# Kernel tuning notes

Hardware: AMD Instinct MI355X
Metric: run time of the kernel (lower is better)

## Reference

```python
import jax, jax.numpy as jnp
import numpy as np

B, T, C, H = 2, 2048, 1024, 16
D = C // H  # head_dim = 64


def setup_inputs() -> dict:
    key = jax.random.key(0)
    ks = jax.random.split(key, 5)
    s = 1.0 / np.sqrt(C)
    return {
        "x": jax.random.normal(ks[0], (B, T, C), jnp.float32),
        "Wq": jax.random.normal(ks[1], (C, C), jnp.float32) * s,
        "bq": jnp.zeros((C,), jnp.float32),
        "Wk": jax.random.normal(ks[2], (C, C), jnp.float32) * s,
        "bk": jnp.zeros((C,), jnp.float32),
        "Wv": jax.random.normal(ks[3], (C, C), jnp.float32) * s,
        "bv": jnp.zeros((C,), jnp.float32),
        "Wo": jax.random.normal(ks[4], (C, C), jnp.float32) * s,
        "bo": jnp.zeros((C,), jnp.float32),
    }


def reference(x, Wq, bq, Wk, bk, Wv, bv, Wo, bo):
    Bx, Tx, Cx = x.shape
    # torch Linear: y = x @ W.T + b
    q = (x @ Wq.T + bq).reshape(Bx, Tx, H, D).transpose(0, 2, 1, 3)  # [B,H,T,D]
    k = (x @ Wk.T + bk).reshape(Bx, Tx, H, D).transpose(0, 2, 1, 3)
    v = (x @ Wv.T + bv).reshape(Bx, Tx, H, D).transpose(0, 2, 1, 3)
    att = jnp.einsum("bhqd,bhkd->bhqk", q, k) / np.sqrt(D).astype(np.float32)
    mask = jnp.tril(jnp.ones((Tx, Tx), bool))  # causal mask [T,T]
    att = jnp.where(mask, att, -jnp.inf)
    att = jax.nn.softmax(att, axis=-1)
    out = jnp.einsum("bhqk,bhkd->bhqd", att, v)
    out = out.transpose(0, 2, 1, 3).reshape(Bx, Tx, Cx)
    return out @ Wo.T + bo
```

## Files before the change

### kernel.cpp

```cpp
#include <hip/hip_runtime.h>
#include <hip/hip_bf16.h>

#define B_ 2
#define T_ 2048
#define C_ 1024
#define H_ 16
#define D_ 64

typedef unsigned short u16;
typedef __bf16 bf16x8 __attribute__((ext_vector_type(8)));
typedef float floatx4 __attribute__((ext_vector_type(4)));

__device__ __forceinline__ float bf2f(u16 u) {
  union { unsigned int i; float f; } x; x.i = ((unsigned int)u) << 16; return x.f;
}
__device__ __forceinline__ u16 f2bf(float f) {
  union { float f; unsigned int i; } x; x.f = f;
  unsigned int r = x.i + 0x7fffu + ((x.i >> 16) & 1u);
  return (u16)(r >> 16);
}

__device__ __forceinline__ unsigned cvtpk(float lo, float hi) {
  unsigned r;
  asm("v_cvt_pk_bf16_f32 %0, %1, %2" : "=v"(r) : "v"(lo), "v"(hi));
  return r;
}

__device__ __forceinline__ void gld16(void* lds, const void* g) {
  __builtin_amdgcn_global_load_lds(
      (const __attribute__((address_space(1))) unsigned int*)g,
      (__attribute__((address_space(3))) unsigned int*)lds, 16, 0, 0);
}

#define NXF4 1048576
#define NWF4 262144

__global__ __launch_bounds__(256) void cvt_all(
    const float* __restrict__ x,  const float* __restrict__ Wq,
    const float* __restrict__ Wk, const float* __restrict__ Wv,
    const float* __restrict__ Wo, u16* __restrict__ dst_base)
{
  const int i = blockIdx.x * 256 + threadIdx.x;
  const float* src; size_t off;
  if (i < NXF4)               { src = x;  off = i; }
  else if (i < NXF4 + NWF4)   { src = Wq; off = i - NXF4; }
  else if (i < NXF4 + 2*NWF4) { src = Wk; off = i - (NXF4 + NWF4); }
  else if (i < NXF4 + 3*NWF4) { src = Wv; off = i - (NXF4 + 2*NWF4); }
  else                        { src = Wo; off = i - (NXF4 + 3*NWF4); }
  float4 f = ((const float4*)src)[off];
  ushort4 o;
  o.x = f2bf(f.x); o.y = f2bf(f.y); o.z = f2bf(f.z); o.w = f2bf(f.w);
  ((ushort4*)dst_base)[i] = o;
}

#define QSCALE 0.1803368801111f

#define PBAR()                                                \
  do {                                                        \
    asm volatile("" ::: "memory");                            \
    __builtin_amdgcn_s_barrier();                             \
    asm volatile("s_waitcnt lgkmcnt(0)" ::: "memory");        \
  } while (0)

#define EBAR()                                                \
  do {                                                        \
    asm volatile("" ::: "memory");                            \
    __builtin_amdgcn_s_barrier();                             \
    asm volatile("" ::: "memory");                            \
  } while (0)

__global__ __launch_bounds__(512, 2) void gemm_qkv8(
    const u16* __restrict__ X, const u16* __restrict__ Wb,
    const float* __restrict__ b0, const float* __restrict__ b1,
    const float* __restrict__ b2,
    u16* __restrict__ Yq, u16* __restrict__ Yk, u16* __restrict__ Yv)
{
  __shared__ __align__(16) u16 L[57344];

  const int tid  = threadIdx.x;
  const int lane = tid & 63;
  const int m16  = lane & 15;
  const int q4   = lane >> 4;
  const int wv   = tid >> 6;
  const int wm   = wv >> 2;
  const int wn   = wv & 3;

  const int bid = blockIdx.x;
  const int xcd = bid & 7;
  const int idx = bid >> 3;
  const int bx  = (xcd & 3) * 4 + (idx & 3);
  const int by  = (xcd >> 2) * 8 + (idx >> 2);

  const u16* Abase  = X  + (size_t)bx * 256 * C_;
  const u16* Bbase  = Wb + (size_t)by * 192 * C_;
  const u16* A1base = Abase + (size_t)128 * C_;

  const int rB  = tid >> 3;
  const int s0 = tid,       r0 = rB;
  const int s1 = tid + 512, r1 = 64 + rB;
  const int k0a = ((tid & 7) ^ (rB & 7)) * 8;

#define STAGE_A(dsthalf, srcrows, kofs)                                       \
  do {                                                                        \
    gld16(&(dsthalf)[s0 * 8], (srcrows) + (size_t)r0 * C_ + (kofs) + k0a);    \
    gld16(&(dsthalf)[s1 * 8], (srcrows) + (size_t)r1 * C_ + (kofs) + k0a);    \
  } while (0)

#define STAGE_BL(dstB, srcrows, kofs, l)                                      \
  gld16(&(dstB)[((l) * 512 + tid) * 8],                                       \
        (srcrows) + (size_t)((l) * 64 + rB) * C_ + (kofs) + k0a)

  u16* buf0 = L;
  u16* buf1 = L + 28672;

  STAGE_BL(buf0 + 16384, Bbase, 0, 0);
  STAGE_BL(buf0 + 16384, Bbase, 0, 1);
  STAGE_BL(buf0 + 16384, Bbase, 0, 2);
  STAGE_A (buf0,         Abase,  0);
  STAGE_A (buf0 + 8192,  A1base, 0);
  STAGE_BL(buf1 + 16384, Bbase, 64, 0);
  STAGE_BL(buf1 + 16384, Bbase, 64, 1);
  STAGE_A (buf1,         Abase, 64);
  asm volatile("s_waitcnt vmcnt(4)" ::: "memory");
  __builtin_amdgcn_s_barrier();
  asm volatile("" ::: "memory");

  floatx4 acc[8][3] = {};

  const int a0off = m16 * 64 + ((q4      ^ (lane & 7)) * 8);
  const int a1off = m16 * 64 + (((q4 + 4) ^ (lane & 7)) * 8);
  const int bro   = wn * 3072;

  for (int i = 0; i < 16; ++i) {
    u16* buf  = (i & 1) ? buf1 : buf0;
    u16* bufn = (i & 1) ? buf0 : buf1;
    const u16* Ah = buf + wm * 8192;
    const u16* Bh = buf + 16384;
    const bool p1 = (i + 1) < 16;
    const bool p2 = (i + 2) < 16;
    const int  k1 = (i + 1) * 64;
    const int  k2 = (i + 2) * 64;

    bf16x8 a[4][2], bA[2][2], bB[2];

#pragma unroll
    for (int f = 0; f < 4; ++f) {
      a[f][0] = *(const bf16x8*)&Ah[f * 1024 + a0off];
      a[f][1] = *(const bf16x8*)&Ah[f * 1024 + a1off];
    }
#pragma unroll
    for (int g = 0; g < 2; ++g) {
      bA[g][0] = *(const bf16x8*)&Bh[bro + g * 1024 + a0off];
      bA[g][1] = *(const bf16x8*)&Bh[bro + g * 1024 + a1off];
    }
    if (p1) STAGE_A(bufn + 8192, A1base, k1);
    PBAR();
    __builtin_amdgcn_s_setprio(1);
#pragma unroll
    for (int f = 0; f < 4; ++f)
#pragma unroll
      for (int g = 0; g < 2; ++g) {
        acc[f][g] = __builtin_amdgcn_mfma_f32_16x16x32_bf16(a[f][0], bA[g][0], acc[f][g], 0, 0, 0);
        acc[f][g] = __builtin_amdgcn_mfma_f32_16x16x32_bf16(a[f][1], bA[g][1], acc[f][g], 0, 0, 0);
      }
    __builtin_amdgcn_s_setprio(0);
    EBAR();

    bB[0] = *(const bf16x8*)&Bh[bro + 2048 + a0off];
    bB[1] = *(const bf16x8*)&Bh[bro + 2048 + a1off];
    if (p1) STAGE_BL(bufn + 16384, Bbase, k1, 2);
    PBAR();
    __builtin_amdgcn_s_setprio(1);
#pragma unroll
    for (int f = 0; f < 4; ++f) {
      acc[f][2] = __builtin_amdgcn_mfma_f32_16x16x32_bf16(a[f][0], bB[0], acc[f][2], 0, 0, 0);
      acc[f][2] = __builtin_amdgcn_mfma_f32_16x16x32_bf16(a[f][1], bB[1], acc[f][2], 0, 0, 0);
    }
    __builtin_amdgcn_s_setprio(0);
    EBAR();

#pragma unroll
    for (int f = 0; f < 4; ++f) {
      a[f][0] = *(const bf16x8*)&Ah[4096 + f * 1024 + a0off];
      a[f][1] = *(const bf16x8*)&Ah[4096 + f * 1024 + a1off];
    }
    if (p2) {
      STAGE_BL(buf + 16384, Bbase, k2, 0);
      STAGE_BL(buf + 16384, Bbase, k2, 1);
    }
    PBAR();
    __builtin_amdgcn_s_setprio(1);
#pragma unroll
    for (int f = 0; f < 4; ++f) {
      acc[4 + f][2] = __builtin_amdgcn_mfma_f32_16x16x32_bf16(a[f][0], bB[0], acc[4 + f][2], 0, 0, 0);
      acc[4 + f][2] = __builtin_amdgcn_mfma_f32_16x16x32_bf16(a[f][1], bB[1], acc[4 + f][2], 0, 0, 0);
    }
    __builtin_amdgcn_s_setprio(0);
    EBAR();

    if (p2) STAGE_A(buf, Abase, k2);
    PBAR();
    __builtin_amdgcn_s_setprio(1);
#pragma unroll
    for (int f = 0; f < 4; ++f)
#pragma unroll
      for (int g = 0; g < 2; ++g) {
        acc[4 + f][g] = __builtin_amdgcn_mfma_f32_16x16x32_bf16(a[f][0], bA[g][0], acc[4 + f][g], 0, 0, 0);
        acc[4 + f][g] = __builtin_amdgcn_mfma_f32_16x16x32_bf16(a[f][1], bA[g][1], acc[4 + f][g], 0, 0, 0);
      }
    __builtin_amdgcn_s_setprio(0);
    asm volatile("" ::: "memory");
    if (p2) asm volatile("s_waitcnt vmcnt(4)" ::: "memory");
    else    asm volatile("s_waitcnt vmcnt(0)" ::: "memory");
    __builtin_amdgcn_s_barrier();
    asm volatile("" ::: "memory");
  }

  const int mbase = bx * 256 + wm * 128 + q4 * 4;
#pragma unroll
  for (int nf = 0; nf < 3; ++nf) {
    const int nzg = by * 192 + wn * 48 + nf * 16 + m16;
    const int z  = nzg >> 10;
    const int nl = nzg & 1023;
    const int h = nl >> 6, d = nl & (D_ - 1);
    const float bv = (z == 0 ? b0 : z == 1 ? b1 : b2)[nl];
    if (z == 2) {
#pragma unroll
      for (int mf = 0; mf < 8; ++mf) {
        const int m  = mbase + mf * 16;
        const int bb = m >> 11, t = m & (T_ - 1);
        ushort4 pk;
        pk.x = f2bf(acc[mf][nf][0] + bv);
        pk.y = f2bf(acc[mf][nf][1] + bv);
        pk.z = f2bf(acc[mf][nf][2] + bv);
        pk.w = f2bf(acc[mf][nf][3] + bv);
        *(ushort4*)&Yv[(((size_t)bb * H_ + h) * D_ + d) * T_ + t] = pk;
      }
    } else {
      u16* Y = z ? Yk : Yq;
      const float sc = z ? 1.0f : QSCALE;
#pragma unroll
      for (int mf = 0; mf < 8; ++mf) {
        const int m  = mbase + mf * 16;
        const int bb = m >> 11, tq = m & (T_ - 1);
#pragma unroll
        for (int r = 0; r < 4; ++r) {
          Y[(((size_t)bb * H_ + h) * T_ + (tq + r)) * D_ + d] =
              f2bf((acc[mf][nf][r] + bv) * sc);
        }
      }
    }
  }
}

__global__ __launch_bounds__(256) void gemm_out(
    const u16* __restrict__ X, const u16* __restrict__ W,
    const float* __restrict__ bias, float* __restrict__ Yf)
{
  const int K = C_, N = C_;
  __shared__ __align__(16) u16 As[128 * 32];
  __shared__ __align__(16) u16 Bs[128 * 32];

  const int tid  = threadIdx.x;
  const int wv   = tid >> 6;
  const int lane = tid & 63;
  const int mcol = lane & 15;
  const int quad = lane >> 4;
  const int wr = wv >> 1, wc = wv & 1;
  const int m0 = blockIdx.x * 128;
  const int n0 = blockIdx.y * 128;

  const int srow = tid >> 2;
  const int scol = (tid & 3) * 8;
  const u16* xp0 = X + (size_t)(m0 + srow) * K + scol;
  const u16* xp1 = xp0 + (size_t)64 * K;
  const u16* wp0 = W + (size_t)(n0 + srow) * K + scol;
  const u16* wp1 = wp0 + (size_t)64 * K;

  floatx4 acc[4][4] = {};

  for (int k0 = 0; k0 < K; k0 += 32) {
    gld16(&As[tid * 8],        xp0 + k0);
    gld16(&As[2048 + tid * 8], xp1 + k0);
    gld16(&Bs[tid * 8],        wp0 + k0);
    gld16(&Bs[2048 + tid * 8], wp1 + k0);
    __syncthreads();

    bf16x8 a[4], b[4];
#pragma unroll
    for (int rf = 0; rf < 4; ++rf)
      a[rf] = *(const bf16x8*)&As[(wr * 64 + rf * 16 + mcol) * 32 + quad * 8];
#pragma unroll
    for (int cf = 0; cf < 4; ++cf)
      b[cf] = *(const bf16x8*)&Bs[(wc * 64 + cf * 16 + mcol) * 32 + quad * 8];
#pragma unroll
    for (int rf = 0; rf < 4; ++rf)
#pragma unroll
      for (int cf = 0; cf < 4; ++cf)
        acc[rf][cf] = __builtin_amdgcn_mfma_f32_16x16x32_bf16(
            a[rf], b[cf], acc[rf][cf], 0, 0, 0);
    __syncthreads();
  }

#pragma unroll
  for (int cf = 0; cf < 4; ++cf) {
    const int n = n0 + wc * 64 + cf * 16 + mcol;
    const float bv = bias[n];
#pragma unroll
    for (int rf = 0; rf < 4; ++rf) {
#pragma unroll
      for (int r = 0; r < 4; ++r) {
        const int m = m0 + wr * 64 + rf * 16 + quad * 4 + r;
        Yf[(size_t)m * N + n] = acc[rf][cf][r] + bv;
      }
    }
  }
}

#define KSB 4096
#define VTB 4096

__global__ __launch_bounds__(256, 5) void attn_flash(
    const u16* __restrict__ Q, const u16* __restrict__ K,
    const u16* __restrict__ Vg, u16* __restrict__ O,
    float* __restrict__ OP, float* __restrict__ LP)
{
  __shared__ __align__(16) u16 Ks[2 * KSB];
  __shared__ __align__(16) u16 Vt[2 * VTB];

  const int tid  = threadIdx.x;
  const int wv   = tid >> 6;
  const int lane = tid & 63;
  const int mcol = lane & 15;
  const int quad = lane >> 4;

  const int bx = blockIdx.x;
  const int bh = bx & 31;
  const int t  = bx >> 5;
  const int iq = (t < 16) ? 31 - t : 47 - t;
  const bool pc = (t < 32);
  const int j0 = (t >= 16 && t < 32) ? 16 : 0;
  const int j1 = (t < 16) ? 15 : iq;
  const int ti = pc ? ((bh * 16 + (iq - 16)) * 2 + (j0 ? 1 : 0)) : 0;

  const size_t base  = (size_t)bh * T_ * D_;
  const size_t vbase = (size_t)bh * D_ * T_;
  const int b = bh >> 4, h = bh & (H_ - 1);

  bf16x8 vones;
  {
    const u16 ov = (mcol == 0) ? (u16)0x3F80 : (u16)0;
    union { u16 s[8]; bf16x8 v; } tmp;
#pragma unroll
    for (int i = 0; i < 8; ++i) tmp.s[i] = ov;
    vones = tmp.v;
  }

  const int srow = lane >> 3;
  const int sg   = (lane & 7) ^ srow;
  const int c0 = wv * 2, c1 = wv * 2 + 1;
  const int sl0 = (quad ^ (mcol & 7)) * 8;

  const size_t koff0 = base + (size_t)(c0 * 8 + srow) * D_ + sg * 8;
  const size_t koff1 = base + (size_t)(c1 * 8 + srow) * D_ + sg * 8;
  const size_t voff0 = vbase + (size_t)(c0 * 8 + srow) * T_ + sg * 8;
  const size_t voff1 = vbase + (size_t)(c1 * 8 + srow) * T_ + sg * 8;

  const u16* qg = Q + base + (size_t)(iq * 64 + wv * 16 + mcol) * D_ + quad * 8;
  const bf16x8 qf0 = *(const bf16x8*)qg;
  const bf16x8 qf1 = *(const bf16x8*)(qg + 32);

  floatx4 oacc[5] = {};

  {
    const size_t kj = (size_t)j0 * 64 * D_;
    const int    vj = j0 * 64;
    gld16(&Ks[c0 * 512 + lane * 8], K  + koff0 + kj);
    gld16(&Ks[c1 * 512 + lane * 8], K  + koff1 + kj);
    gld16(&Vt[c0 * 512 + lane * 8], Vg + voff0 + vj);
    gld16(&Vt[c1 * 512 + lane * 8], Vg + voff1 + vj);
  }

  for (int j = j0; j <= j1; ++j) {
    const int cur = (j - j0) & 1;
    __syncthreads();

    if (j < j1) {
      const int nb = cur ^ 1;
      const size_t kj = (size_t)(j + 1) * 64 * D_;
      const int    vj = (j + 1) * 64;
      gld16(&Ks[nb * KSB + c0 * 512 + lane * 8], K  + koff0 + kj);
      gld16(&Ks[nb * KSB + c1 * 512 + lane * 8], K  + koff1 + kj);
      gld16(&Vt[nb * VTB + c0 * 512 + lane * 8], Vg + voff0 + vj);
      gld16(&Vt[nb * VTB + c1 * 512 + lane * 8], Vg + voff1 + vj);
    }

    const u16* ksb = &Ks[cur * KSB];
    const u16* vtb = &Vt[cur * VTB];

    floatx4 sacc[4] = {};
#pragma unroll
    for (int nt = 0; nt < 4; ++nt) {
      const u16* kr = &ksb[(nt * 16 + mcol) * 64];
      bf16x8 kb0 = *(const bf16x8*)&kr[sl0];
      bf16x8 kb1 = *(const bf16x8*)&kr[sl0 ^ 32];
      sacc[nt] = __builtin_amdgcn_mfma_f32_16x16x32_bf16(kb0, qf0, sacc[nt], 0, 0, 0);
      sacc[nt] = __builtin_amdgcn_mfma_f32_16x16x32_bf16(kb1, qf1, sacc[nt], 0, 0, 0);
    }

    if (j == iq) {
      const int ql = wv * 16 + mcol;
#pragma unroll
      for (int nt = 0; nt < 4; ++nt) {
#pragma unroll
        for (int r = 0; r < 4; ++r)
          if (nt * 16 + quad * 4 + r > ql) sacc[nt][r] = -1e30f;
      }
    }

    unsigned w0[2], w1[2], w2[2], w3[2];
#pragma unroll
    for (int i = 0; i < 2; ++i) {
      w0[i] = cvtpk(exp2f(sacc[0][2*i]), exp2f(sacc[0][2*i+1]));
      w1[i] = cvtpk(exp2f(sacc[1][2*i]), exp2f(sacc[1][2*i+1]));
      w2[i] = cvtpk(exp2f(sacc[2][2*i]), exp2f(sacc[2][2*i+1]));
      w3[i] = cvtpk(exp2f(sacc[3][2*i]), exp2f(sacc[3][2*i+1]));
    }

    union { unsigned u[4]; bf16x8 v; } pa0u, pa1u;
#pragma unroll
    for (int i = 0; i < 2; ++i) {
      unsigned x = w0[i], y = w1[i];
      asm("v_permlane32_swap_b32 %0, %1" : "+v"(x), "+v"(y));
      asm("v_permlane16_swap_b32 %0, %1" : "+v"(x), "+v"(y));
      pa0u.u[i] = x; pa0u.u[i + 2] = y;
      unsigned x2 = w2[i], y2 = w3[i];
      asm("v_permlane32_swap_b32 %0, %1" : "+v"(x2), "+v"(y2));
      asm("v_permlane16_swap_b32 %0, %1" : "+v"(x2), "+v"(y2));
      pa1u.u[i] = x2; pa1u.u[i + 2] = y2;
    }
    const bf16x8 pa0 = pa0u.v;
    const bf16x8 pa1 = pa1u.v;

#pragma unroll
    for (int dt = 0; dt < 4; ++dt) {
      const u16* vr = &vtb[(dt * 16 + mcol) * 64];
      bf16x8 vb0 = *(const bf16x8*)&vr[sl0];
      bf16x8 vb1 = *(const bf16x8*)&vr[sl0 ^ 32];
      oacc[dt] = __builtin_amdgcn_mfma_f32_16x16x32_bf16(pa0, vb0, oacc[dt], 0, 0, 0);
      oacc[dt] = __builtin_amdgcn_mfma_f32_16x16x32_bf16(pa1, vb1, oacc[dt], 0, 0, 0);
    }
    oacc[4] = __builtin_amdgcn_mfma_f32_16x16x32_bf16(pa0, vones, oacc[4], 0, 0, 0);
    oacc[4] = __builtin_amdgcn_mfma_f32_16x16x32_bf16(pa1, vones, oacc[4], 0, 0, 0);
  }

  if (!pc) {
    float invl[4];
#pragma unroll
    for (int r = 0; r < 4; ++r)
      invl[r] = 1.f / __shfl(oacc[4][r], lane & 48);
#pragma unroll
    for (int dt = 0; dt < 4; ++dt) {
      const int c = h * D_ + dt * 16 + mcol;
#pragma unroll
      for (int r = 0; r < 4; ++r) {
        const int tg = iq * 64 + wv * 16 + quad * 4 + r;
        O[((size_t)b * T_ + tg) * C_ + c] = f2bf(oacc[dt][r] * invl[r]);
      }
    }
  } else {
    float* op = OP + (size_t)ti * 4096;
#pragma unroll
    for (int dt = 0; dt < 4; ++dt)
#pragma unroll
      for (int r = 0; r < 4; ++r)
        op[(wv * 16 + quad * 4 + r) * 64 + dt * 16 + mcol] = oacc[dt][r];
    if (mcol == 0) {
#pragma unroll
      for (int r = 0; r < 4; ++r)
        LP[ti * 64 + wv * 16 + quad * 4 + r] = oacc[4][r];
    }
  }
}

__global__ __launch_bounds__(256) void attn_merge(
    const float* __restrict__ OP, const float* __restrict__ LP,
    u16* __restrict__ O)
{
  const int mb = blockIdx.x;
  const int bh = mb & 31, qt = mb >> 5;
  const int iq = 16 + qt;
  const int ti0 = (bh * 16 + qt) * 2;
  const int b = bh >> 4, h = bh & (H_ - 1);
  const int row = threadIdx.x >> 2;
  const int dc  = (threadIdx.x & 3) * 16;

  const float l = LP[ti0 * 64 + row] + LP[(ti0 + 1) * 64 + row];
  const float inv = 1.f / l;
  const float* pa = OP + (size_t)ti0 * 4096 + row * 64 + dc;
  const float* pb = pa + 4096;

  const int tg = iq * 64 + row;
  u16* o = O + ((size_t)b * T_ + tg) * C_ + h * D_ + dc;

  u16 tmp[16];
#pragma unroll
  for (int i = 0; i < 4; ++i) {
    const float4 a4 = ((const float4*)pa)[i];
    const float4 b4 = ((const float4*)pb)[i];
    tmp[i*4 + 0] = f2bf((a4.x + b4.x) * inv);
    tmp[i*4 + 1] = f2bf((a4.y + b4.y) * inv);
    tmp[i*4 + 2] = f2bf((a4.z + b4.z) * inv);
    tmp[i*4 + 3] = f2bf((a4.w + b4.w) * inv);
  }
  *(uint4*)&o[0] = *(const uint4*)&tmp[0];
  *(uint4*)&o[8] = *(const uint4*)&tmp[8];
}

extern "C" void kernel_launch(void* const* d_in, const int* in_sizes, int n_in,
                              void* d_out, int out_size, void* d_ws, size_t ws_size,
                              hipStream_t stream) {
  const float* x  = (const float*)d_in[0];
  const float* Wq = (const float*)d_in[1];
  const float* bq = (const float*)d_in[2];
  const float* Wk = (const float*)d_in[3];
  const float* bk = (const float*)d_in[4];
  const float* Wv = (const float*)d_in[5];
  const float* bv = (const float*)d_in[6];
  const float* Wo = (const float*)d_in[7];
  const float* bo = (const float*)d_in[8];
  float* out = (float*)d_out;

  const size_t NX = (size_t)B_ * T_ * C_;
  const size_t NW = (size_t)C_ * C_;

  u16* xb  = (u16*)d_ws;
  u16* wqb = xb  + NX;
  u16* wkb = wqb + NW;
  u16* wvb = wkb + NW;
  u16* wob = wvb + NW;
  u16* q   = wob + NW;
  u16* k   = q   + NX;
  u16* v   = k   + NX;
  u16* ctx = v   + NX;
  float* opart = (float*)(ctx + NX);
  float* lpart = opart + (size_t)1024 * 4096;

  cvt_all<<<dim3((NXF4 + 4 * NWF4) / 256), 256, 0, stream>>>(x, Wq, Wk, Wv, Wo, xb);

  gemm_qkv8<<<dim3(256), 512, 0, stream>>>(xb, wqb, bq, bk, bv, q, k, v);

  attn_flash<<<dim3(1536), 256, 0, stream>>>(q, k, v, ctx, opart, lpart);

  attn_merge<<<dim3(512), 256, 0, stream>>>(opart, lpart, ctx);

  gemm_out<<<dim3(32, 8), 256, 0, stream>>>(ctx, wob, bo, out);
}
```

Baseline: 183.6 us.

## Enlarge attention query tile to 128 rows with table-driven causal split scheduling

Each attention block now handles 128 query rows, two 16-row sub-tiles per wave, so every K/V tile staged in shared memory feeds twice as many MFMAs. This halves K/V load and barrier traffic per unit of work. A constant lookup table assigns each of 24 chunk slots a query tile and key range, splitting long causal rows into two partials merged later, and the merge kernel is adjusted to match. MFMA sections are wrapped in s_setprio, and occupancy hints drop to 3 blocks per SM, which raises register pressure and shortens the grid to 768 blocks.

```diff
diff --git a/kernel.cpp b/kernel.cpp
--- a/kernel.cpp
+++ b/kernel.cpp
@@ -320,7 +320,12 @@
 #define KSB 4096
 #define VTB 4096
 
-__global__ __launch_bounds__(256, 5) void attn_flash(
+__constant__ unsigned char CH_T[24]  = {7,15,15,14,14,6,13,13, 4,10,10,5,11,11,12,12, 9,9,8,8,3,2,1,0};
+__constant__ unsigned char CH_J0[24] = {0,0,16,0,15,0,0,14,   0,0,11,0,0,12,0,13,    0,10,0,9,0,0,0,0};
+__constant__ unsigned char CH_J1[24] = {15,15,31,14,29,13,13,27, 9,10,21,11,11,23,12,25, 9,19,8,17,7,5,3,1};
+__constant__ unsigned char CH_P[24]  = {0,1,2,1,2,0,1,2,      0,1,2,0,1,2,1,2,       1,2,1,2,0,0,0,0};
+
+__global__ __launch_bounds__(256, 3) void attn_flash(
     const u16* __restrict__ Q, const u16* __restrict__ K,
     const u16* __restrict__ Vg, u16* __restrict__ O,
     float* __restrict__ OP, float* __restrict__ LP)
@@ -336,12 +341,12 @@
 
   const int bx = blockIdx.x;
   const int bh = bx & 31;
-  const int t  = bx >> 5;
-  const int iq = (t < 16) ? 31 - t : 47 - t;
-  const bool pc = (t < 32);
-  const int j0 = (t >= 16 && t < 32) ? 16 : 0;
-  const int j1 = (t < 16) ? 15 : iq;
-  const int ti = pc ? ((bh * 16 + (iq - 16)) * 2 + (j0 ? 1 : 0)) : 0;
+  const int c  = bx >> 5;
+  const int t  = CH_T[c];
+  const int j0 = CH_J0[c];
+  const int j1 = CH_J1[c];
+  const int pm = CH_P[c];
+  const int ti = pm ? ((bh * 8 + (t - 8)) * 2 + (pm - 1)) : 0;
 
   const size_t base  = (size_t)bh * T_ * D_;
   const size_t vbase = (size_t)bh * D_ * T_;
@@ -366,11 +371,13 @@
   const size_t voff0 = vbase + (size_t)(c0 * 8 + srow) * T_ + sg * 8;
   const size_t voff1 = vbase + (size_t)(c1 * 8 + srow) * T_ + sg * 8;
 
-  const u16* qg = Q + base + (size_t)(iq * 64 + wv * 16 + mcol) * D_ + quad * 8;
-  const bf16x8 qf0 = *(const bf16x8*)qg;
-  const bf16x8 qf1 = *(const bf16x8*)(qg + 32);
-
-  floatx4 oacc[5] = {};
+  const u16* qg = Q + base + (size_t)(t * 128 + wv * 32 + mcol) * D_ + quad * 8;
+  const bf16x8 qf[2][2] = {
+    { *(const bf16x8*)qg,             *(const bf16x8*)(qg + 32) },
+    { *(const bf16x8*)(qg + 16 * D_), *(const bf16x8*)(qg + 16 * D_ + 32) }
+  };
+
+  floatx4 oacc[2][5] = {};
 
   {
     const size_t kj = (size_t)j0 * 64 * D_;
@@ -398,87 +405,106 @@
     const u16* ksb = &Ks[cur * KSB];
     const u16* vtb = &Vt[cur * VTB];
 
-    floatx4 sacc[4] = {};
+    floatx4 sacc[2][4] = {};
+    __builtin_amdgcn_s_setprio(1);
 #pragma unroll
     for (int nt = 0; nt < 4; ++nt) {
       const u16* kr = &ksb[(nt * 16 + mcol) * 64];
       bf16x8 kb0 = *(const bf16x8*)&kr[sl0];
       bf16x8 kb1 = *(const bf16x8*)&kr[sl0 ^ 32];
-      sacc[nt] = __builtin_amdgcn_mfma_f32_16x16x32_bf16(kb0, qf0, sacc[nt], 0, 0, 0);
-      sacc[nt] = __builtin_amdgcn_mfma_f32_16x16x32_bf16(kb1, qf1, sacc[nt], 0, 0, 0);
-    }
-
-    if (j == iq) {
-      const int ql = wv * 16 + mcol;
-#pragma unroll
-      for (int nt = 0; nt < 4; ++nt) {
-#pragma unroll
-        for (int r = 0; r < 4; ++r)
-          if (nt * 16 + quad * 4 + r > ql) sacc[nt][r] = -1e30f;
-      }
-    }
-
-    unsigned w0[2], w1[2], w2[2], w3[2];
-#pragma unroll
-    for (int i = 0; i < 2; ++i) {
-      w0[i] = cvtpk(exp2f(sacc[0][2*i]), exp2f(sacc[0][2*i+1]));
-      w1[i] = cvtpk(exp2f(sacc[1][2*i]), exp2f(sacc[1][2*i+1]));
-      w2[i] = cvtpk(exp2f(sacc[2][2*i]), exp2f(sacc[2][2*i+1]));
-      w3[i] = cvtpk(exp2f(sacc[3][2*i]), exp2f(sacc[3][2*i+1]));
-    }
-
-    union { unsigned u[4]; bf16x8 v; } pa0u, pa1u;
-#pragma unroll
-    for (int i = 0; i < 2; ++i) {
-      unsigned x = w0[i], y = w1[i];
-      asm("v_permlane32_swap_b32 %0, %1" : "+v"(x), "+v"(y));
-      asm("v_permlane16_swap_b32 %0, %1" : "+v"(x), "+v"(y));
-      pa0u.u[i] = x; pa0u.u[i + 2] = y;
-      unsigned x2 = w2[i], y2 = w3[i];
-      asm("v_permlane32_swap_b32 %0, %1" : "+v"(x2), "+v"(y2));
-      asm("v_permlane16_swap_b32 %0, %1" : "+v"(x2), "+v"(y2));
-      pa1u.u[i] = x2; pa1u.u[i + 2] = y2;
-    }
-    const bf16x8 pa0 = pa0u.v;
-    const bf16x8 pa1 = pa1u.v;
-
+      sacc[0][nt] = __builtin_amdgcn_mfma_f32_16x16x32_bf16(kb0, qf[0][0], sacc[0][nt], 0, 0, 0);
+      sacc[0][nt] = __builtin_amdgcn_mfma_f32_16x16x32_bf16(kb1, qf[0][1], sacc[0][nt], 0, 0, 0);
+      sacc[1][nt] = __builtin_amdgcn_mfma_f32_16x16x32_bf16(kb0, qf[1][0], sacc[1][nt], 0, 0, 0);
+      sacc[1][nt] = __builtin_amdgcn_mfma_f32_16x16x32_bf16(kb1, qf[1][1], sacc[1][nt], 0, 0, 0);
+    }
+    __builtin_amdgcn_s_setprio(0);
+
+    const int dj = j - 2 * t;
+    if (dj >= 0) {
+#pragma unroll
+      for (int hf = 0; hf < 2; ++hf) {
+        const int klim = wv * 32 + hf * 16 + mcol - dj * 64;
+#pragma unroll
+        for (int nt = 0; nt < 4; ++nt)
+#pragma unroll
+          for (int r = 0; r < 4; ++r)
+            if (nt * 16 + quad * 4 + r > klim) sacc[hf][nt][r] = -1e30f;
+      }
+    }
+
+    bf16x8 pa[2][2];
+#pragma unroll
+    for (int hf = 0; hf < 2; ++hf) {
+      unsigned w[4][2];
+#pragma unroll
+      for (int nt = 0; nt < 4; ++nt)
+#pragma unroll
+        for (int i = 0; i < 2; ++i)
+          w[nt][i] = cvtpk(exp2f(sacc[hf][nt][2*i]), exp2f(sacc[hf][nt][2*i+1]));
+      union { unsigned u[4]; bf16x8 v; } p0, p1;
+#pragma unroll
+      for (int i = 0; i < 2; ++i) {
+        unsigned x = w[0][i], y = w[1][i];
+        asm("v_permlane32_swap_b32 %0, %1" : "+v"(x), "+v"(y));
+        asm("v_permlane16_swap_b32 %0, %1" : "+v"(x), "+v"(y));
+        p0.u[i] = x; p0.u[i + 2] = y;
+        unsigned x2 = w[2][i], y2 = w[3][i];
+        asm("v_permlane32_swap_b32 %0, %1" : "+v"(x2), "+v"(y2));
+        asm("v_permlane16_swap_b32 %0, %1" : "+v"(x2), "+v"(y2));
+        p1.u[i] = x2; p1.u[i + 2] = y2;
+      }
+      pa[hf][0] = p0.v; pa[hf][1] = p1.v;
+    }
+
+    __builtin_amdgcn_s_setprio(1);
 #pragma unroll
     for (int dt = 0; dt < 4; ++dt) {
       const u16* vr = &vtb[(dt * 16 + mcol) * 64];
       bf16x8 vb0 = *(const bf16x8*)&vr[sl0];
       bf16x8 vb1 = *(const bf16x8*)&vr[sl0 ^ 32];
-      oacc[dt] = __builtin_amdgcn_mfma_f32_16x16x32_bf16(pa0, vb0, oacc[dt], 0, 0, 0);
-      oacc[dt] = __builtin_amdgcn_mfma_f32_16x16x32_bf16(pa1, vb1, oacc[dt], 0, 0, 0);
-    }
-    oacc[4] = __builtin_amdgcn_mfma_f32_16x16x32_bf16(pa0, vones, oacc[4], 0, 0, 0);
-    oacc[4] = __builtin_amdgcn_mfma_f32_16x16x32_bf16(pa1, vones, oacc[4], 0, 0, 0);
-  }
-
-  if (!pc) {
-    float invl[4];
-#pragma unroll
-    for (int r = 0; r < 4; ++r)
-      invl[r] = 1.f / __shfl(oacc[4][r], lane & 48);
-#pragma unroll
-    for (int dt = 0; dt < 4; ++dt) {
-      const int c = h * D_ + dt * 16 + mcol;
-#pragma unroll
-      for (int r = 0; r < 4; ++r) {
-        const int tg = iq * 64 + wv * 16 + quad * 4 + r;
-        O[((size_t)b * T_ + tg) * C_ + c] = f2bf(oacc[dt][r] * invl[r]);
+      oacc[0][dt] = __builtin_amdgcn_mfma_f32_16x16x32_bf16(pa[0][0], vb0, oacc[0][dt], 0, 0, 0);
+      oacc[0][dt] = __builtin_amdgcn_mfma_f32_16x16x32_bf16(pa[0][1], vb1, oacc[0][dt], 0, 0, 0);
+      oacc[1][dt] = __builtin_amdgcn_mfma_f32_16x16x32_bf16(pa[1][0], vb0, oacc[1][dt], 0, 0, 0);
+      oacc[1][dt] = __builtin_amdgcn_mfma_f32_16x16x32_bf16(pa[1][1], vb1, oacc[1][dt], 0, 0, 0);
+    }
+    oacc[0][4] = __builtin_amdgcn_mfma_f32_16x16x32_bf16(pa[0][0], vones, oacc[0][4], 0, 0, 0);
+    oacc[0][4] = __builtin_amdgcn_mfma_f32_16x16x32_bf16(pa[0][1], vones, oacc[0][4], 0, 0, 0);
+    oacc[1][4] = __builtin_amdgcn_mfma_f32_16x16x32_bf16(pa[1][0], vones, oacc[1][4], 0, 0, 0);
+    oacc[1][4] = __builtin_amdgcn_mfma_f32_16x16x32_bf16(pa[1][1], vones, oacc[1][4], 0, 0, 0);
+    __builtin_amdgcn_s_setprio(0);
+  }
+
+  if (!pm) {
+#pragma unroll
+    for (int hf = 0; hf < 2; ++hf) {
+      float invl[4];
+#pragma unroll
+      for (int r = 0; r < 4; ++r)
+        invl[r] = 1.f / __shfl(oacc[hf][4][r], lane & 48);
+#pragma unroll
+      for (int dt = 0; dt < 4; ++dt) {
+        const int cc = h * D_ + dt * 16 + mcol;
+#pragma unroll
+        for (int r = 0; r < 4; ++r) {
+          const int tg = t * 128 + wv * 32 + hf * 16 + quad * 4 + r;
+          O[((size_t)b * T_ + tg) * C_ + cc] = f2bf(oacc[hf][dt][r] * invl[r]);
+        }
       }
     }
   } else {
-    float* op = OP + (size_t)ti * 4096;
-#pragma unroll
-    for (int dt = 0; dt < 4; ++dt)
-#pragma unroll
-      for (int r = 0; r < 4; ++r)
-        op[(wv * 16 + quad * 4 + r) * 64 + dt * 16 + mcol] = oacc[dt][r];
-    if (mcol == 0) {
-#pragma unroll
-      for (int r = 0; r < 4; ++r)
-        LP[ti * 64 + wv * 16 + quad * 4 + r] = oacc[4][r];
+    float* op = OP + (size_t)ti * 8192;
+#pragma unroll
+    for (int hf = 0; hf < 2; ++hf) {
+#pragma unroll
+      for (int dt = 0; dt < 4; ++dt)
+#pragma unroll
+        for (int r = 0; r < 4; ++r)
+          op[(wv * 32 + hf * 16 + quad * 4 + r) * 64 + dt * 16 + mcol] = oacc[hf][dt][r];
+      if (mcol == 0) {
+#pragma unroll
+        for (int r = 0; r < 4; ++r)
+          LP[ti * 128 + wv * 32 + hf * 16 + quad * 4 + r] = oacc[hf][4][r];
+      }
     }
   }
 }
@@ -488,24 +514,24 @@
     u16* __restrict__ O)
 {
   const int mb = blockIdx.x;
-  const int bh = mb & 31, qt = mb >> 5;
-  const int iq = 16 + qt;
-  const int ti0 = (bh * 16 + qt) * 2;
+  const int bh = mb & 31, tt = mb >> 5;
+  const int t = 8 + tt;
+  const int ti0 = (bh * 8 + tt) * 2;
   const int b = bh >> 4, h = bh & (H_ - 1);
-  const int row = threadIdx.x >> 2;
-  const int dc  = (threadIdx.x & 3) * 16;
-
-  const float l = LP[ti0 * 64 + row] + LP[(ti0 + 1) * 64 + row];
+  const int row = threadIdx.x >> 1;
+  const int dc  = (threadIdx.x & 1) * 32;
+
+  const float l = LP[ti0 * 128 + row] + LP[(ti0 + 1) * 128 + row];
   const float inv = 1.f / l;
-  const float* pa = OP + (size_t)ti0 * 4096 + row * 64 + dc;
-  const float* pb = pa + 4096;
-
-  const int tg = iq * 64 + row;
+  const float* pa = OP + (size_t)ti0 * 8192 + row * 64 + dc;
+  const float* pb = pa + 8192;
+
+  const int tg = t * 128 + row;
   u16* o = O + ((size_t)b * T_ + tg) * C_ + h * D_ + dc;
 
-  u16 tmp[16];
-#pragma unroll
-  for (int i = 0; i < 4; ++i) {
+  u16 tmp[32];
+#pragma unroll
+  for (int i = 0; i < 8; ++i) {
     const float4 a4 = ((const float4*)pa)[i];
     const float4 b4 = ((const float4*)pb)[i];
     tmp[i*4 + 0] = f2bf((a4.x + b4.x) * inv);
@@ -513,8 +539,9 @@
     tmp[i*4 + 2] = f2bf((a4.z + b4.z) * inv);
     tmp[i*4 + 3] = f2bf((a4.w + b4.w) * inv);
   }
-  *(uint4*)&o[0] = *(const uint4*)&tmp[0];
-  *(uint4*)&o[8] = *(const uint4*)&tmp[8];
+#pragma unroll
+  for (int i = 0; i < 4; ++i)
+    ((uint4*)o)[i] = ((const uint4*)tmp)[i];
 }
 
 extern "C" void kernel_launch(void* const* d_in, const int* in_sizes, int n_in,
@@ -544,15 +571,15 @@
   u16* v   = k   + NX;
   u16* ctx = v   + NX;
   float* opart = (float*)(ctx + NX);
-  float* lpart = opart + (size_t)1024 * 4096;
+  float* lpart = opart + (size_t)512 * 8192;
 
   cvt_all<<<dim3((NXF4 + 4 * NWF4) / 256), 256, 0, stream>>>(x, Wq, Wk, Wv, Wo, xb);
 
   gemm_qkv8<<<dim3(256), 512, 0, stream>>>(xb, wqb, bq, bk, bv, q, k, v);
 
-  attn_flash<<<dim3(1536), 256, 0, stream>>>(q, k, v, ctx, opart, lpart);
-
-  attn_merge<<<dim3(512), 256, 0, stream>>>(opart, lpart, ctx);
+  attn_flash<<<dim3(768), 256, 0, stream>>>(q, k, v, ctx, opart, lpart);
+
+  attn_merge<<<dim3(256), 256, 0, stream>>>(opart, lpart, ctx);
 
   gemm_out<<<dim3(32, 8), 256, 0, stream>>>(ctx, wob, bo, out);
 }
```

Measured after the change: 185.4 us. About the same (+1.0%).
